# Kernel optimization log

Hardware: AMD Instinct MI355X
Metric: run time of the kernel (lower is better)

Reference implementation:

```python
import jax, jax.numpy as jnp
import numpy as np

N_QUBITS = 20
SUPPORT = (3, 8, 15)   # qubit_support
BATCH = 8
DIM = 2 ** len(SUPPORT)  # 8


def setup_inputs() -> dict:
    key = jax.random.key(0)
    ks = jax.random.split(key, 5)
    state_shape = (2,) * N_QUBITS + (BATCH,)
    state_real = jax.random.normal(ks[0], state_shape, dtype=jnp.float32)
    state_imag = jax.random.normal(ks[1], state_shape, dtype=jnp.float32)
    a = jax.random.normal(ks[2], (DIM, DIM), dtype=jnp.float32)
    b = jax.random.normal(ks[3], (DIM, DIM), dtype=jnp.float32)
    h_real = ((a + a.T) * 0.5)[..., None]   # (DIM, DIM, 1) symmetric
    h_imag = ((b - b.T) * 0.5)[..., None]   # antisymmetric -> H Hermitian
    t = jax.random.uniform(ks[4], (BATCH,), dtype=jnp.float32)
    return {"state_real": state_real, "state_imag": state_imag,
            "h_real": h_real, "h_imag": h_imag, "t": t}


def reference(state_real, state_imag, h_real, h_imag, t):
    # state: (2,)*N_QUBITS + (BATCH,) complex
    state = state_real + 1j * state_imag
    # Hermitian generator, hmat layout (d, d, batch_h=1) as in the module buffer
    H = (h_real + 1j * h_imag)[..., 0]                      # (DIM, DIM)
    # _unitary: expm(-1j * t * H) per batch. H Hermitian -> exact via eigh.
    w, V = jnp.linalg.eigh(H)                               # w real (DIM,), V (DIM, DIM)
    phases = jnp.exp(-1j * (t[:, None] * w[None, :]))       # (BATCH, DIM)
    U = jnp.einsum('ik,bk,jk->bij', V, phases, V.conj())    # (BATCH, DIM, DIM)
    # apply_operator: reshape U into per-qubit indices and contract at SUPPORT axes
    s = len(SUPPORT)
    op = U.reshape((BATCH,) + (2,) * (2 * s))               # (B, out bits..., in bits...)
    B_LBL = 100
    out_lbls = [200 + i for i in range(s)]
    op_axes = [B_LBL] + out_lbls + list(SUPPORT)
    state_axes = list(range(N_QUBITS)) + [B_LBL]
    out_axes = list(range(N_QUBITS))
    for i, q in enumerate(SUPPORT):
        out_axes[q] = out_lbls[i]
    out_axes = out_axes + [B_LBL]
    return jnp.einsum(op, op_axes, state, state_axes, out_axes)
```

## Files before the change

kernel.cpp:

```cpp
#include <hip/hip_runtime.h>


#define SUP_OFF(m) ( ((m)&4 ? 524288u : 0u) + ((m)&2 ? 16384u : 0u) + ((m)&1 ? 128u : 0u) )

__global__ void expm_kernel(const float* __restrict__ h_real,
                            const float* __restrict__ h_imag,
                            const float* __restrict__ t_g,
                            float* __restrict__ U)
{
    __shared__ float Tre[64], Tim[64], Mre[64], Mim[64], Ere[64], Eim[64];

    const int b = blockIdx.x;
    const int e = threadIdx.x;
    const int o = e >> 3, i = e & 7;

    const float sc  = t_g[b] * (1.0f / 32.0f);
    const float mre =  sc * h_imag[e];
    const float mim = -sc * h_real[e];

    Mre[e] = mre; Mim[e] = mim;
    Tre[e] = mre; Tim[e] = mim;
    float are = (o == i ? 1.f : 0.f) + mre;
    float aim = mim;
    __syncthreads();

    for (int k = 2; k <= 10; ++k) {
        float sre = 0.f, sim = 0.f;
        #pragma unroll
        for (int j = 0; j < 8; ++j) {
            const float tre = Tre[o * 8 + j], tim = Tim[o * 8 + j];
            const float qre = Mre[j * 8 + i], qim = Mim[j * 8 + i];
            sre += tre * qre - tim * qim;
            sim += tre * qim + tim * qre;
        }
        const float inv = 1.0f / (float)k;
        sre *= inv; sim *= inv;
        __syncthreads();
        Tre[e] = sre; Tim[e] = sim;
        are += sre; aim += sim;
        __syncthreads();
    }

    Ere[e] = are; Eim[e] = aim;
    __syncthreads();

    for (int sq = 0; sq < 5; ++sq) {
        float sre = 0.f, sim = 0.f;
        #pragma unroll
        for (int j = 0; j < 8; ++j) {
            const float xre = Ere[o * 8 + j], xim = Eim[o * 8 + j];
            const float yre = Ere[j * 8 + i], yim = Eim[j * 8 + i];
            sre += xre * yre - xim * yim;
            sim += xre * yim + xim * yre;
        }
        __syncthreads();
        if (sq < 4) {
            Ere[e] = sre; Eim[e] = sim;
            __syncthreads();
        } else {
            U[(i * 8 + b) * 16 + 2 * o]     = sre;
            U[(i * 8 + b) * 16 + 2 * o + 1] = sim;
        }
    }
}

__global__ __launch_bounds__(256, 7) void apply_kernel(
        const float* __restrict__ sre_g,
        const float* __restrict__ sim_g,
        const float4* __restrict__ U4,
        float* __restrict__ out)
{
    __shared__ alignas(16) float ldsRe[2048];
    __shared__ alignas(16) float ldsIm[2048];
    __shared__ alignas(16) float uL[8 * 8 * 20];

    const int tid = threadIdx.x;

    {
        const float4 u = U4[tid];
        const int ib = tid >> 2, k = tid & 3;
        *(float4*)&uL[ib * 20 + k * 4] = u;
    }

    const unsigned B = blockIdx.x;
    const unsigned addr_hi = ((B & 0x1Fu)  << 9)
                           | ((B & 0x1E0u) << 10)
                           | ((B & 0xE00u) << 11);

    #pragma unroll
    for (int c = 0; c < 4; ++c) {
        const unsigned gbase = addr_hi + ((c & 2) ? 524288u : 0u)
                                       + ((c & 1) ? 16384u  : 0u);
        *(float2*)&ldsRe[c * 512 + tid * 2] = *(const float2*)(sre_g + gbase + tid * 2);
        *(float2*)&ldsIm[c * 512 + tid * 2] = *(const float2*)(sim_g + gbase + tid * 2);
    }
    __syncthreads();

    const int l  = tid & 127;
    const int rb = tid >> 7;
    const int b  = l & 7;
    const int xbase = rb * 256 + l;

    float acc[8];
    #pragma unroll
    for (int o = 0; o < 8; ++o) acc[o] = 0.f;

    #pragma unroll
    for (int i = 0; i < 8; ++i) {
        const int xoff = (i >> 1) * 512 + (i & 1) * 128 + xbase;
        const float xr = ldsRe[xoff];
        const float xi = ldsIm[xoff];
        const float4* uv = (const float4*)&uL[(i * 8 + b) * 20];
        const float4 u01 = uv[0], u23 = uv[1], u45 = uv[2], u67 = uv[3];
        acc[0] += u01.x * xr - u01.y * xi;
        acc[1] += u01.z * xr - u01.w * xi;
        acc[2] += u23.x * xr - u23.y * xi;
        acc[3] += u23.z * xr - u23.w * xi;
        acc[4] += u45.x * xr - u45.y * xi;
        acc[5] += u45.z * xr - u45.w * xi;
        acc[6] += u67.x * xr - u67.y * xi;
        acc[7] += u67.z * xr - u67.w * xi;
    }
    __syncthreads();

    #pragma unroll
    for (int o = 0; o < 8; ++o) {
        ldsRe[(o >> 1) * 512 + (o & 1) * 128 + xbase] = acc[o];
    }
    __syncthreads();

    #pragma unroll
    for (int c = 0; c < 4; ++c) {
        const unsigned gbase = addr_hi + ((c & 2) ? 524288u : 0u)
                                       + ((c & 1) ? 16384u  : 0u);
        *(float2*)(out + gbase + tid * 2) = *(const float2*)&ldsRe[c * 512 + tid * 2];
    }
}

extern "C" void kernel_launch(void* const* d_in, const int* in_sizes, int n_in,
                              void* d_out, int out_size, void* d_ws, size_t ws_size,
                              hipStream_t stream) {
    const float* state_real = (const float*)d_in[0];
    const float* state_imag = (const float*)d_in[1];
    const float* h_real     = (const float*)d_in[2];
    const float* h_imag     = (const float*)d_in[3];
    const float* t          = (const float*)d_in[4];

    float* U = (float*)d_ws;

    expm_kernel<<<8, 64, 0, stream>>>(h_real, h_imag, t, U);

    apply_kernel<<<4096, 256, 0, stream>>>(state_real, state_imag,
                                           (const float4*)U, (float*)d_out);
}
```

Measured before the change: 26.27 us.

## Software-pipeline apply kernel over four tiles per block with register prefetch

The apply kernel now launches 1024 blocks of 512 threads, and each block walks four consecutive sub-tiles. It prefetches the next tile's state into registers while computing the current one, and uses float4 global loads and stores. Each thread computes four of the eight outputs instead of eight, and a separate output LDS buffer is added. This is meant to hide global load latency and amortize the U staging per block. In exchange it adds more barriers per block and more LDS use, which could lower occupancy.

Result: no change. 26.73 us (+1.8%).

```diff
diff --git a/kernel.cpp b/kernel.cpp
--- a/kernel.cpp
+++ b/kernel.cpp
@@ -1,7 +1,8 @@
 #include <hip/hip_runtime.h>
 
 
-#define SUP_OFF(m) ( ((m)&4 ? 524288u : 0u) + ((m)&2 ? 16384u : 0u) + ((m)&1 ? 128u : 0u) )
+#define CQ3 524288u
+#define CQ8 16384u
 
 __global__ void expm_kernel(const float* __restrict__ h_real,
                             const float* __restrict__ h_imag,
@@ -64,76 +65,78 @@
     }
 }
 
-__global__ __launch_bounds__(256, 7) void apply_kernel(
+__global__ __launch_bounds__(512, 8) void apply_kernel(
         const float* __restrict__ sre_g,
         const float* __restrict__ sim_g,
         const float4* __restrict__ U4,
         float* __restrict__ out)
 {
-    __shared__ alignas(16) float ldsRe[2048];
-    __shared__ alignas(16) float ldsIm[2048];
+    __shared__ alignas(16) float inRe[4 * 512];
+    __shared__ alignas(16) float inIm[4 * 512];
+    __shared__ alignas(16) float outL[4 * 512];
     __shared__ alignas(16) float uL[8 * 8 * 20];
 
     const int tid = threadIdx.x;
+    const unsigned B = blockIdx.x;
+    const unsigned addr_hi = ((B & 0x007u) << 11)
+                           | ((B & 0x078u) << 12)
+                           | ((B & 0x380u) << 13);
 
-    {
+    const int c = tid >> 7;
+    const int j = tid & 127;
+    const unsigned cOff = ((c & 2) ? CQ3 : 0u) + ((c & 1) ? CQ8 : 0u);
+    const unsigned gchunk = addr_hi + cOff;
+
+    float4 rRe = *(const float4*)(sre_g + gchunk + j * 4);
+    float4 rIm = *(const float4*)(sim_g + gchunk + j * 4);
+
+    if (tid < 256) {
         const float4 u = U4[tid];
         const int ib = tid >> 2, k = tid & 3;
         *(float4*)&uL[ib * 20 + k * 4] = u;
     }
 
-    const unsigned B = blockIdx.x;
-    const unsigned addr_hi = ((B & 0x1Fu)  << 9)
-                           | ((B & 0x1E0u) << 10)
-                           | ((B & 0xE00u) << 11);
-
-    #pragma unroll
-    for (int c = 0; c < 4; ++c) {
-        const unsigned gbase = addr_hi + ((c & 2) ? 524288u : 0u)
-                                       + ((c & 1) ? 16384u  : 0u);
-        *(float2*)&ldsRe[c * 512 + tid * 2] = *(const float2*)(sre_g + gbase + tid * 2);
-        *(float2*)&ldsIm[c * 512 + tid * 2] = *(const float2*)(sim_g + gbase + tid * 2);
-    }
-    __syncthreads();
-
     const int l  = tid & 127;
-    const int rb = tid >> 7;
+    const int rb = (tid >> 7) & 1;
+    const int h  = tid >> 8;
     const int b  = l & 7;
     const int xbase = rb * 256 + l;
 
-    float acc[8];
     #pragma unroll
-    for (int o = 0; o < 8; ++o) acc[o] = 0.f;
+    for (int n = 0; n < 4; ++n) {
+        *(float4*)&inRe[c * 512 + j * 4] = rRe;
+        *(float4*)&inIm[c * 512 + j * 4] = rIm;
+        __syncthreads();
 
-    #pragma unroll
-    for (int i = 0; i < 8; ++i) {
-        const int xoff = (i >> 1) * 512 + (i & 1) * 128 + xbase;
-        const float xr = ldsRe[xoff];
-        const float xi = ldsIm[xoff];
-        const float4* uv = (const float4*)&uL[(i * 8 + b) * 20];
-        const float4 u01 = uv[0], u23 = uv[1], u45 = uv[2], u67 = uv[3];
-        acc[0] += u01.x * xr - u01.y * xi;
-        acc[1] += u01.z * xr - u01.w * xi;
-        acc[2] += u23.x * xr - u23.y * xi;
-        acc[3] += u23.z * xr - u23.w * xi;
-        acc[4] += u45.x * xr - u45.y * xi;
-        acc[5] += u45.z * xr - u45.w * xi;
-        acc[6] += u67.x * xr - u67.y * xi;
-        acc[7] += u67.z * xr - u67.w * xi;
-    }
-    __syncthreads();
+        if (n < 3) {
+            rRe = *(const float4*)(sre_g + gchunk + (n + 1) * 512 + j * 4);
+            rIm = *(const float4*)(sim_g + gchunk + (n + 1) * 512 + j * 4);
+        }
 
-    #pragma unroll
-    for (int o = 0; o < 8; ++o) {
-        ldsRe[(o >> 1) * 512 + (o & 1) * 128 + xbase] = acc[o];
-    }
-    __syncthreads();
+        float a0 = 0.f, a1 = 0.f, a2 = 0.f, a3 = 0.f;
+        #pragma unroll
+        for (int i = 0; i < 8; ++i) {
+            const int xoff = (i >> 1) * 512 + (i & 1) * 128 + xbase;
+            const float xr = inRe[xoff];
+            const float xi = inIm[xoff];
+            const float4* uv = (const float4*)&uL[(i * 8 + b) * 20];
+            const float4 uA = uv[2 * h];
+            const float4 uB = uv[2 * h + 1];
+            a0 += uA.x * xr - uA.y * xi;
+            a1 += uA.z * xr - uA.w * xi;
+            a2 += uB.x * xr - uB.y * xi;
+            a3 += uB.z * xr - uB.w * xi;
+        }
 
-    #pragma unroll
-    for (int c = 0; c < 4; ++c) {
-        const unsigned gbase = addr_hi + ((c & 2) ? 524288u : 0u)
-                                       + ((c & 1) ? 16384u  : 0u);
-        *(float2*)(out + gbase + tid * 2) = *(const float2*)&ldsRe[c * 512 + tid * 2];
+        const int o0 = 4 * h;
+        outL[((o0    ) >> 1) * 512 + ((o0    ) & 1) * 128 + xbase] = a0;
+        outL[((o0 + 1) >> 1) * 512 + ((o0 + 1) & 1) * 128 + xbase] = a1;
+        outL[((o0 + 2) >> 1) * 512 + ((o0 + 2) & 1) * 128 + xbase] = a2;
+        outL[((o0 + 3) >> 1) * 512 + ((o0 + 3) & 1) * 128 + xbase] = a3;
+        __syncthreads();
+
+        *(float4*)(out + gchunk + n * 512 + j * 4) =
+            *(const float4*)&outL[c * 512 + j * 4];
     }
 }
 
@@ -150,6 +153,6 @@
 
     expm_kernel<<<8, 64, 0, stream>>>(h_real, h_imag, t, U);
 
-    apply_kernel<<<4096, 256, 0, stream>>>(state_real, state_imag,
+    apply_kernel<<<1024, 512, 0, stream>>>(state_real, state_imag,
                                            (const float4*)U, (float*)d_out);
 }
```
